# Kernel optimization log

Measured on AMD Instinct MI355X. Metric: run time of the kernel, lower is better.

## Reference

```python
import jax, jax.numpy as jnp
import numpy as np

# static architecture constants (match init_kwargs)
H, D, N_BASIS, MEM_LEN, QLEN = 16, 128, 1024, 512, 2048
RIDGE = 0.5
BASIS_SIGMAS = (0.005, 0.01)


def _gaussian_pdf(x, mu, sigma):
    return jnp.exp(-0.5 * ((x - mu) / sigma) ** 2) / (sigma * jnp.sqrt(2.0 * jnp.pi))


def _basis_params(n):
    # torch.meshgrid(linspace(0,1,n//2), sigmas, indexing='ij') then flatten
    m = jnp.linspace(0.0, 1.0, n // len(BASIS_SIGMAS)).astype(jnp.float32)
    mu = jnp.repeat(m, len(BASIS_SIGMAS))
    sigma = jnp.tile(jnp.asarray(BASIS_SIGMAS, jnp.float32), n // len(BASIS_SIGMAS))
    return mu, sigma


def _compute_G(l, b_mu, b_sigma, n):
    # padded linear positions on [-0.5+shift, 1.5-shift], l even -> 2l points
    shift = 1.0 / (2 * l)
    pos = jnp.linspace(-0.5 + shift, 1.5 - shift, 2 * l).astype(jnp.float32)
    F = _gaussian_pdf(pos[None, :], b_mu[:, None], b_sigma[:, None])  # [N, 2l]
    # G = F^T (F F^T + ridge I)^{-1}, then crop padding rows -> [l, N]
    G = jnp.linalg.solve(F @ F.T + RIDGE * jnp.eye(n, dtype=jnp.float32), F).T
    return G[l // 2: -(l // 2)]


def _forward(k, q, W_key, W_val, W_out, w_mu, w_sigma):
    d = H * D
    b_mu, b_sigma = _basis_params(N_BASIS)
    k = k[:, -512:, :]                                   # forward truncates memory
    l = k.shape[1]
    G = _compute_G(l, b_mu, b_sigma, N_BASIS)            # [l, N]
    # value_function: project signal onto basis coefficients B -> [1, N, d]
    B = jnp.einsum('bld,ln->bnd', k, G)
    keys = (B @ W_key.T).reshape(1, N_BASIS, H, D).transpose(0, 2, 1, 3)    # [1,H,N,D]
    values = (B @ W_val.T).reshape(1, N_BASIS, H, D).transpose(0, 2, 1, 3)  # [1,H,N,D]
    scores = jnp.einsum('bhqd,bhnd->bhqn', q / jnp.sqrt(jnp.float32(D)), keys)
    mu = jax.nn.sigmoid(scores @ w_mu)[..., None]                           # [1,H,Q,1]
    sigma_sq = jnp.maximum(jax.nn.softplus(scores @ w_sigma), 1e-4)[..., None]
    # continuous softmax over Gaussian RBFs: r_j = E_{t~N(mu,sigma_sq)}[psi_j(t)]
    # closed form: N(mu; b_mu_j, sigma_sq + b_sigma_j^2)
    r = _gaussian_pdf(b_mu, mu, jnp.sqrt(sigma_sq + b_sigma ** 2))          # [1,H,Q,N]
    context = jnp.einsum('bhqn,bhnd->bqhd', r, values).reshape(1, QLEN, d)
    return context @ W_out.T


def setup_inputs() -> dict:
    key = jax.random.key(0)
    ks = jax.random.split(key, 7)
    d = H * D
    s = 0.02
    return {
        'k': jax.random.normal(ks[0], (1, MEM_LEN, d), jnp.float32),
        'q': jax.random.normal(ks[1], (1, H, QLEN, D), jnp.float32),
        'W_key': jax.random.normal(ks[2], (d, d), jnp.float32) * s,
        'W_val': jax.random.normal(ks[3], (d, d), jnp.float32) * s,
        'W_out': jax.random.normal(ks[4], (d, d), jnp.float32) * s,
        'w_mu': jax.random.normal(ks[5], (N_BASIS,), jnp.float32) * s,
        'w_sigma': jax.random.normal(ks[6], (N_BASIS,), jnp.float32) * s,
        'new_doc': 1,
    }


def reference(k, q, W_key, W_val, W_out, w_mu, w_sigma, new_doc):
    # new_doc=True -> B_past/x_past reset, so only the fresh-memory path runs
    return _forward(k, q, W_key, W_val, W_out, w_mu, w_sigma)
```

## Files before the change

kernel.cpp:

```cpp
#include <hip/hip_runtime.h>
#include <hip/hip_bf16.h>
#include <vector>
#include <cmath>
#include <cstring>

using bf16 = __hip_bfloat16;
typedef short s16x8 __attribute__((ext_vector_type(8)));
typedef float f32x4 __attribute__((ext_vector_type(4)));

static constexpr int kH = 16, kD = 128, kNB = 1024, kML = 512, kQL = 2048, kDM = 2048;

#define VMB(N) do { asm volatile("s_waitcnt vmcnt(" #N ")" ::: "memory"); \
                    __builtin_amdgcn_s_barrier(); \
                    asm volatile("" ::: "memory"); } while (0)
#define VMLB(N) do { asm volatile("s_waitcnt vmcnt(" #N ") lgkmcnt(0)" ::: "memory"); \
                     __builtin_amdgcn_s_barrier(); \
                     asm volatile("" ::: "memory"); } while (0)
#define SWZ(c) ((c) ^ (((c) >> 4) & 3))

static void compute_Gt_host(float* Gt) {
  const int n = kNB, P = 2 * kML;
  std::vector<double> F((size_t)n * P), A((size_t)n * n), pos(P);
  const double shift = 1.0 / (double)P;
  const double p0 = -0.5 + shift, p1 = 1.5 - shift;
  for (int i = 0; i < P; i++) pos[i] = p0 + (p1 - p0) * (double)i / (double)(P - 1);
  const double c0 = 0.3989422804014327;
  std::vector<int> lo(n), hi(n);
  for (int b = 0; b < n; b++) {
    double mu = (double)(b >> 1) / 511.0;
    double sg = (b & 1) ? 0.01 : 0.005;
    double c = c0 / sg;
    double* Fb = &F[(size_t)b * P];
    for (int i = 0; i < P; i++) { double t = (pos[i] - mu) / sg; Fb[i] = c * exp(-0.5 * t * t); }
    int l = 0; while (l < P - 1 && pos[l] < mu - 14.0 * sg) l++;
    int h = P - 1; while (h > 0 && pos[h] > mu + 14.0 * sg) h--;
    lo[b] = l; hi[b] = h;
  }
  for (int i = 0; i < n; i++) {
    const double* fi = &F[(size_t)i * P];
    for (int j = 0; j <= i; j++) {
      const double* fj = &F[(size_t)j * P];
      int a = lo[i] > lo[j] ? lo[i] : lo[j];
      int b2 = hi[i] < hi[j] ? hi[i] : hi[j];
      double s = 0.0;
      for (int k2 = a; k2 <= b2; k2++) s += fi[k2] * fj[k2];
      A[(size_t)i * n + j] = s;
      if (i != j) A[(size_t)j * n + i] = s;
    }
    A[(size_t)i * n + i] += 0.5;
  }
  for (int j = 0; j < n; j++) {
    double* Aj = &A[(size_t)j * n];
    double d = Aj[j];
    for (int k2 = 0; k2 < j; k2++) d -= Aj[k2] * Aj[k2];
    d = std::sqrt(d); Aj[j] = d;
    double inv = 1.0 / d;
    for (int i = j + 1; i < n; i++) {
      double* Ai = &A[(size_t)i * n];
      double s = Ai[j];
      for (int k2 = 0; k2 < j; k2++) s -= Ai[k2] * Aj[k2];
      Ai[j] = s * inv;
    }
  }
  for (int i = 0; i < n; i++) {
    double* yi = &F[(size_t)i * P];
    const double* Ai = &A[(size_t)i * n];
    for (int k2 = 0; k2 < i; k2++) {
      double lik = Ai[k2];
      const double* yk = &F[(size_t)k2 * P];
      for (int t = 0; t < P; t++) yi[t] -= lik * yk[t];
    }
    double inv = 1.0 / Ai[i];
    for (int t = 0; t < P; t++) yi[t] *= inv;
  }
  for (int i = n - 1; i >= 0; i--) {
    double* xi = &F[(size_t)i * P];
    for (int k2 = i + 1; k2 < n; k2++) {
      double lki = A[(size_t)k2 * n + i];
      const double* xk = &F[(size_t)k2 * P];
      for (int t = 0; t < P; t++) xi[t] -= lki * xk[t];
    }
    double inv = 1.0 / A[(size_t)i * n + i];
    for (int t = 0; t < P; t++) xi[t] *= inv;
  }
  for (int b = 0; b < n; b++)
    for (int l = 0; l < kML; l++)
      Gt[(size_t)b * kML + l] = (float)F[(size_t)b * P + (kML / 2) + l];
}

static unsigned short f2bf_host(float x) {
  unsigned u; std::memcpy(&u, &x, 4);
  unsigned r = (u + 0x7FFFu + ((u >> 16) & 1u)) >> 16;
  return (unsigned short)r;
}
static float bf2f_host(unsigned short b) {
  unsigned u = ((unsigned)b) << 16; float f; std::memcpy(&f, &u, 4); return f;
}

namespace {
struct Init {
  float* d_GtTf = nullptr;
  unsigned short* d_Gth = nullptr;
  unsigned short* d_Gtl = nullptr;
  float* h_GtTf_pinned = nullptr;
  unsigned short* h_Gth_pinned = nullptr;
  unsigned short* h_Gtl_pinned = nullptr;
  std::vector<float> h_GtTf;
  std::vector<unsigned short> h_Gth, h_Gtl;
  Init() {
    std::vector<float> h_Gt((size_t)kNB * kML);
    compute_Gt_host(h_Gt.data());
    h_GtTf.resize(h_Gt.size());
    h_Gth.resize(h_Gt.size());
    h_Gtl.resize(h_Gt.size());
    for (int n = 0; n < kNB; n++)
      for (int l = 0; l < kML; l++) {
        float v = h_Gt[(size_t)n * kML + l];
        h_GtTf[(size_t)l * kNB + n] = v;
        unsigned short hb = f2bf_host(v);
        h_Gth[(size_t)n * kML + l] = hb;
        h_Gtl[(size_t)n * kML + l] = f2bf_host(v - bf2f_host(hb));
      }
    const size_t fb = h_Gt.size() * 4, bb = h_Gt.size() * 2;
    if (hipMalloc((void**)&d_GtTf, fb) == hipSuccess) {
      if (hipMemcpy(d_GtTf, h_GtTf.data(), fb, hipMemcpyHostToDevice) != hipSuccess) { hipFree(d_GtTf); d_GtTf = nullptr; }
    }
    if (hipMalloc((void**)&d_Gth, bb) == hipSuccess) {
      if (hipMemcpy(d_Gth, h_Gth.data(), bb, hipMemcpyHostToDevice) != hipSuccess) { hipFree(d_Gth); d_Gth = nullptr; }
    }
    if (hipMalloc((void**)&d_Gtl, bb) == hipSuccess) {
      if (hipMemcpy(d_Gtl, h_Gtl.data(), bb, hipMemcpyHostToDevice) != hipSuccess) { hipFree(d_Gtl); d_Gtl = nullptr; }
    }
    if (!d_GtTf && hipHostMalloc((void**)&h_GtTf_pinned, fb, 0) == hipSuccess)
      std::memcpy(h_GtTf_pinned, h_GtTf.data(), fb);
    if (!d_Gth && hipHostMalloc((void**)&h_Gth_pinned, bb, 0) == hipSuccess)
      std::memcpy(h_Gth_pinned, h_Gth.data(), bb);
    if (!d_Gtl && hipHostMalloc((void**)&h_Gtl_pinned, bb, 0) == hipSuccess)
      std::memcpy(h_Gtl_pinned, h_Gtl.data(), bb);
  }
};
Init g_init;
}

__device__ inline short f2bf(float x) {
  unsigned u = __float_as_uint(x);
  unsigned r = (u + 0x7FFFu + ((u >> 16) & 1u)) >> 16;
  return (short)r;
}
__device__ inline float bf2f(short b) {
  return __uint_as_float(((unsigned)(unsigned short)b) << 16);
}

__device__ inline void gload16(const void* g, void* l) {
  __builtin_amdgcn_global_load_lds(
      (__attribute__((address_space(1))) void*)(g),
      (__attribute__((address_space(3))) void*)(l),
      16, 0, 0);
}

__global__ __launch_bounds__(256) void detect_kernel(const unsigned short* __restrict__ q,
                                                     int* __restrict__ flag) {
  int t = threadIdx.x;
  int bad = 0;
  for (int i = t; i < 4096; i += 256) {
    int e = (q[i] >> 7) & 0xFF;
    if (e >= 0x98) bad = 1;
  }
  __shared__ int s[256];
  s[t] = bad; __syncthreads();
  for (int k2 = 128; k2 > 0; k2 >>= 1) { if (t < k2) s[t] |= s[t + k2]; __syncthreads(); }
  if (t == 0) *flag = s[0];
}

__global__ __launch_bounds__(256) void conv_bf16(const void* __restrict__ in,
                                                 short* __restrict__ out, int n4,
                                                 const int* __restrict__ flag) {
  int i = blockIdx.x * 256 + threadIdx.x;
  if (i >= n4) return;
  if (*flag) {
    float4 v = ((const float4*)in)[i];
    short4 o; o.x = f2bf(v.x); o.y = f2bf(v.y); o.z = f2bf(v.z); o.w = f2bf(v.w);
    ((short4*)out)[i] = o;
  } else {
    ((short4*)out)[i] = ((const short4*)in)[i];
  }
}

__global__ __launch_bounds__(256) void gw_kernel(const float* __restrict__ GtT,
                                                 const void* __restrict__ wmu,
                                                 const void* __restrict__ wsg,
                                                 float* __restrict__ gw,
                                                 const int* __restrict__ flag) {
  const bool f32 = (*flag != 0);
  const int l = blockIdx.x, t = threadIdx.x;
  const float* row = GtT + (long long)l * kNB;
  float a = 0.f, b = 0.f;
  for (int n = t; n < kNB; n += 256) {
    float g = row[n];
    float wm_ = f32 ? ((const float*)wmu)[n] : bf2f(((const short*)wmu)[n]);
    float ws_ = f32 ? ((const float*)wsg)[n] : bf2f(((const short*)wsg)[n]);
    a += g * wm_; b += g * ws_;
  }
  __shared__ float red[2][256];
  red[0][t] = a; red[1][t] = b;
  __syncthreads();
  for (int s = 128; s > 0; s >>= 1) {
    if (t < s) { red[0][t] += red[0][t + s]; red[1][t] += red[1][t + s]; }
    __syncthreads();
  }
  if (t == 0) { gw[l] = red[0][0]; gw[kML + l] = red[1][0]; }
}

__global__ __launch_bounds__(256) void bwk_kernel(const void* __restrict__ kin,
                                                  const float* __restrict__ gw,
                                                  float* __restrict__ bw,
                                                  const int* __restrict__ flag) {
  const bool f32 = (*flag != 0);
  int j = blockIdx.x * 256 + threadIdx.x;
  int l0 = blockIdx.y * 32;
  float a = 0.f, b = 0.f;
  for (int l = l0; l < l0 + 32; l++) {
    float kv = f32 ? ((const float*)kin)[(long long)l * kDM + j]
                   : bf2f(((const short*)kin)[(long long)l * kDM + j]);
    a += kv * gw[l]; b += kv * gw[kML + l];
  }
  atomicAdd(&bw[j], a);
  atomicAdd(&bw[kDM + j], b);
}

__global__ __launch_bounds__(256) void kw_kernel(const void* __restrict__ Wk,
                                                 const float* __restrict__ bw,
                                                 float* __restrict__ kw,
                                                 const int* __restrict__ flag) {
  const bool f32 = (*flag != 0);
  int i = blockIdx.x;
  float smu = 0.f, ssg = 0.f;
  if (f32) {
    const float* row = (const float*)Wk + (long long)i * kDM;
    for (int j = threadIdx.x; j < kDM; j += 256) { float w = row[j]; smu += w * bw[j]; ssg += w * bw[kDM + j]; }
  } else {
    const short* row = (const short*)Wk + (long long)i * kDM;
    for (int j = threadIdx.x; j < kDM; j += 256) { float w = bf2f(row[j]); smu += w * bw[j]; ssg += w * bw[kDM + j]; }
  }
  __shared__ float red[2][256];
  red[0][threadIdx.x] = smu; red[1][threadIdx.x] = ssg;
  __syncthreads();
  for (int s = 128; s > 0; s >>= 1) {
    if (threadIdx.x < (unsigned)s) {
      red[0][threadIdx.x] += red[0][threadIdx.x + s];
      red[1][threadIdx.x] += red[1][threadIdx.x + s];
    }
    __syncthreads();
  }
  if (threadIdx.x == 0) { kw[i] = red[0][0]; kw[kDM + i] = red[1][0]; }
}

__global__ __launch_bounds__(256) void musig_kernel(const void* __restrict__ q,
                                                    const float* __restrict__ kw,
                                                    float* __restrict__ mu,
                                                    float* __restrict__ sigsq,
                                                    const int* __restrict__ flag) {
  const bool f32 = (*flag != 0);
  int w = threadIdx.x >> 6, lane = threadIdx.x & 63;
  int idx = blockIdx.x * 4 + w;
  int h = idx >> 11;
  const float* kmu = kw + h * kD;
  const float* ksg = kw + kDM + h * kD;
  float q0, q1;
  if (f32) {
    const float* qrow = (const float*)q + (long long)idx * kD;
    q0 = qrow[lane]; q1 = qrow[lane + 64];
  } else {
    const short* qrow = (const short*)q + (long long)idx * kD;
    q0 = bf2f(qrow[lane]); q1 = bf2f(qrow[lane + 64]);
  }
  float a = q0 * kmu[lane] + q1 * kmu[lane + 64];
  float b = q0 * ksg[lane] + q1 * ksg[lane + 64];
  for (int s = 32; s > 0; s >>= 1) { a += __shfl_xor(a, s); b += __shfl_xor(b, s); }
  if (lane == 0) {
    const float inv_sqrt_d = 0.08838834764831845f;
    float zm = a * inv_sqrt_d, zs = b * inv_sqrt_d;
    mu[idx] = 1.f / (1.f + __expf(-zm));
    float sp = (zs > 20.f) ? zs : log1pf(__expf(zs));
    sigsq[idx] = fmaxf(sp, 1e-4f);
  }
}

template <int CSTORE>
__global__ __launch_bounds__(256) void mfma_gemm_bt(
    const short* __restrict__ A0, int lda, long long sA,
    const short* __restrict__ BT0, int ldb, long long sB,
    void* __restrict__ C0, int ldc, long long sC,
    int K, const int* __restrict__ flag) {
  __shared__ s16x8 lA[3][1024];
  __shared__ s16x8 lB[3][512];
  const short* A = A0 + (long long)blockIdx.z * sA;
  const short* BT = BT0 + (long long)blockIdx.z * sB;
  const int t = threadIdx.x;
  const int wave = t >> 6, lane = t & 63;
  const int quad = lane >> 4, l16 = lane & 15;
  const int wm = wave >> 1, wn = wave & 1;
  const int m0 = blockIdx.y * 128, n0 = blockIdx.x * 64;
  const int srow = lane & 15, skc = lane >> 4;
  auto stage = [&](int b, int kk) {
#pragma unroll
    for (int i = 0; i < 2; i++) {
      int sub = wave + i * 4;
      int m = sub * 16 + srow;
#pragma unroll
      for (int ks = 0; ks < 2; ks++)
        gload16(A + (long long)(m0 + m) * lda + kk + ks * 32 + skc * 8,
                &lA[b][ks * 512 + sub * 64]);
    }
    int mB = wave * 16 + srow;
#pragma unroll
    for (int ks = 0; ks < 2; ks++)
      gload16(BT + (long long)(n0 + mB) * ldb + kk + ks * 32 + skc * 8,
              &lB[b][ks * 256 + wave * 64]);
  };
  f32x4 acc[4][2];
  const f32x4 z = {0.f, 0.f, 0.f, 0.f};
#pragma unroll
  for (int i = 0; i < 4; i++)
#pragma unroll
    for (int j = 0; j < 2; j++) acc[i][j] = z;
  stage(0, 0);
  stage(1, 64);
  VMB(6);
  const int NT = K >> 6;
  int cur = 0, pf = 2;
  for (int tt = 0; tt < NT; ++tt) {
    const bool more = (tt + 2 < NT);
    if (more) stage(pf, (tt + 2) << 6);
#pragma unroll
    for (int ks = 0; ks < 2; ks++) {
      s16x8 af[4], bfr[2];
#pragma unroll
      for (int i = 0; i < 4; i++) af[i] = lA[cur][ks * 512 + (wm * 4 + i) * 64 + lane];
#pragma unroll
      for (int j = 0; j < 2; j++) bfr[j] = lB[cur][ks * 256 + (wn * 2 + j) * 64 + lane];
#pragma unroll
      for (int i = 0; i < 4; i++)
#pragma unroll
        for (int j = 0; j < 2; j++)
          acc[i][j] = __builtin_amdgcn_mfma_f32_16x16x32_bf16(af[i], bfr[j], acc[i][j], 0, 0, 0);
    }
    if (more) VMB(6); else VMB(0);
    cur = (cur == 2) ? 0 : cur + 1;
    pf = (pf == 2) ? 0 : pf + 1;
  }
  if (CSTORE == 0) {
    short* Cp = (short*)C0 + (long long)blockIdx.z * sC;
#pragma unroll
    for (int i = 0; i < 4; i++)
#pragma unroll
      for (int j = 0; j < 2; j++) {
        int gn = n0 + (wn * 2 + j) * 16 + l16;
#pragma unroll
        for (int rg = 0; rg < 4; rg++) {
          int gm = m0 + (wm * 4 + i) * 16 + quad * 4 + rg;
          Cp[(long long)gm * ldc + gn] = f2bf(acc[i][j][rg]);
        }
      }
  } else {
    if (*flag) {
      float* Cp = (float*)C0 + (long long)blockIdx.z * sC;
#pragma unroll
      for (int i = 0; i < 4; i++)
#pragma unroll
        for (int j = 0; j < 2; j++) {
          int gn = n0 + (wn * 2 + j) * 16 + l16;
#pragma unroll
          for (int rg = 0; rg < 4; rg++) {
            int gm = m0 + (wm * 4 + i) * 16 + quad * 4 + rg;
            Cp[(long long)gm * ldc + gn] = acc[i][j][rg];
          }
        }
    } else {
      short* Cp = (short*)C0 + (long long)blockIdx.z * sC;
#pragma unroll
      for (int i = 0; i < 4; i++)
#pragma unroll
        for (int j = 0; j < 2; j++) {
          int gn = n0 + (wn * 2 + j) * 16 + l16;
#pragma unroll
          for (int rg = 0; rg < 4; rg++) {
            int gm = m0 + (wm * 4 + i) * 16 + quad * 4 + rg;
            Cp[(long long)gm * ldc + gn] = f2bf(acc[i][j][rg]);
          }
        }
    }
  }
}

__global__ __launch_bounds__(256) void mfma_gemm_sk(
    const short* __restrict__ A0, int lda,
    const short* __restrict__ BT0, int ldb,
    float* __restrict__ P, int ldc) {
  __shared__ s16x8 lA[3][1024], lB[3][512];
  const int t = threadIdx.x;
  const int wave = t >> 6, lane = t & 63;
  const int quad = lane >> 4, l16 = lane & 15;
  const int wm = wave >> 1, wn = wave & 1;
  const int m0 = blockIdx.y * 128, n0 = blockIdx.x * 64;
  const int kbeg = blockIdx.z * 512;
  const int srow = lane & 15, skc = lane >> 4;
  auto stage = [&](int b, int kk) {
#pragma unroll
    for (int i = 0; i < 2; i++) {
      int sub = wave + i * 4;
      int m = sub * 16 + srow;
#pragma unroll
      for (int ks = 0; ks < 2; ks++)
        gload16(A0 + (long long)(m0 + m) * lda + kk + ks * 32 + skc * 8,
                &lA[b][ks * 512 + sub * 64]);
    }
    int mB = wave * 16 + srow;
#pragma unroll
    for (int ks = 0; ks < 2; ks++)
      gload16(BT0 + (long long)(n0 + mB) * ldb + kk + ks * 32 + skc * 8,
              &lB[b][ks * 256 + wave * 64]);
  };
  f32x4 acc[4][2];
  const f32x4 z = {0.f, 0.f, 0.f, 0.f};
#pragma unroll
  for (int i = 0; i < 4; i++)
#pragma unroll
    for (int j = 0; j < 2; j++) acc[i][j] = z;
  stage(0, kbeg);
  stage(1, kbeg + 64);
  VMB(6);
  const int NT = 8;
  int cur = 0, pf = 2;
  for (int tt = 0; tt < NT; ++tt) {
    const bool more = (tt + 2 < NT);
    if (more) stage(pf, kbeg + ((tt + 2) << 6));
#pragma unroll
    for (int ks = 0; ks < 2; ks++) {
      s16x8 af[4], bfr[2];
#pragma unroll
      for (int i = 0; i < 4; i++) af[i] = lA[cur][ks * 512 + (wm * 4 + i) * 64 + lane];
#pragma unroll
      for (int j = 0; j < 2; j++) bfr[j] = lB[cur][ks * 256 + (wn * 2 + j) * 64 + lane];
#pragma unroll
      for (int i = 0; i < 4; i++)
#pragma unroll
        for (int j = 0; j < 2; j++)
          acc[i][j] = __builtin_amdgcn_mfma_f32_16x16x32_bf16(af[i], bfr[j], acc[i][j], 0, 0, 0);
    }
    if (more) VMB(6); else VMB(0);
    cur = (cur == 2) ? 0 : cur + 1;
    pf = (pf == 2) ? 0 : pf + 1;
  }
  float* Cp = P + (long long)blockIdx.z * kML * kDM;
#pragma unroll
  for (int i = 0; i < 4; i++)
#pragma unroll
    for (int j = 0; j < 2; j++) {
      int gn = n0 + (wn * 2 + j) * 16 + l16;
#pragma unroll
      for (int rg = 0; rg < 4; rg++) {
        int gm = m0 + (wm * 4 + i) * 16 + quad * 4 + rg;
        Cp[(long long)gm * ldc + gn] = acc[i][j][rg];
      }
    }
}

__global__ __launch_bounds__(256) void reduceT_kernel(const float* __restrict__ P,
                                                      short* __restrict__ kvT) {
  __shared__ float tile[64][65];
  const int bd = blockIdx.x, bl = blockIdx.y;
  const int tx = threadIdx.x & 63, ty = threadIdx.x >> 6;
  for (int i = ty; i < 64; i += 4) {
    int l = bl * 64 + i, d = bd * 64 + tx;
    float s = 0.f;
#pragma unroll
    for (int z = 0; z < 4; z++) s += P[((long long)z * kML + l) * kDM + d];
    tile[i][tx] = s;
  }
  __syncthreads();
  for (int i = ty; i < 64; i += 4) {
    int d = bd * 64 + i, l = bl * 64 + tx;
    kvT[(long long)d * kML + l] = f2bf(tile[tx][i]);
  }
}

__global__ __launch_bounds__(256) void mfma_gemm_bt2(
    const short* __restrict__ A0, int lda,
    const short* __restrict__ BTh, const short* __restrict__ BTl, int ldb,
    short* __restrict__ Ch, short* __restrict__ Cl, int ldc, int K) {
  __shared__ s16x8 lA[3][256], lBh[3][256], lBl[3][256];
  const int t = threadIdx.x;
  const int wave = t >> 6, lane = t & 63;
  const int quad = lane >> 4, l16 = lane & 15;
  const int wm = wave >> 1, wn = wave & 1;
  const int m0 = blockIdx.y * 64, n0 = blockIdx.x * 64;
  const int srow = lane & 15, skc = lane >> 4;
  auto stage = [&](int b, int kk) {
    int m = wave * 16 + srow;
    gload16(A0 + (long long)(m0 + m) * lda + kk + skc * 8, &lA[b][wave * 64]);
    gload16(BTh + (long long)(n0 + m) * ldb + kk + skc * 8, &lBh[b][wave * 64]);
    gload16(BTl + (long long)(n0 + m) * ldb + kk + skc * 8, &lBl[b][wave * 64]);
  };
  f32x4 acc[2][2];
  const f32x4 z = {0.f, 0.f, 0.f, 0.f};
#pragma unroll
  for (int i = 0; i < 2; i++)
#pragma unroll
    for (int j = 0; j < 2; j++) acc[i][j] = z;
  stage(0, 0);
  stage(1, 32);
  VMB(3);
  const int NT = K >> 5;
  int cur = 0, pf = 2;
  for (int tt = 0; tt < NT; ++tt) {
    const bool more = (tt + 2 < NT);
    if (more) stage(pf, (tt + 2) << 5);
    s16x8 af[2], bh[2], bl[2];
#pragma unroll
    for (int i = 0; i < 2; i++) af[i] = lA[cur][(wm * 2 + i) * 64 + lane];
#pragma unroll
    for (int j = 0; j < 2; j++) {
      bh[j] = lBh[cur][(wn * 2 + j) * 64 + lane];
      bl[j] = lBl[cur][(wn * 2 + j) * 64 + lane];
    }
#pragma unroll
    for (int i = 0; i < 2; i++)
#pragma unroll
      for (int j = 0; j < 2; j++) {
        acc[i][j] = __builtin_amdgcn_mfma_f32_16x16x32_bf16(af[i], bh[j], acc[i][j], 0, 0, 0);
        acc[i][j] = __builtin_amdgcn_mfma_f32_16x16x32_bf16(af[i], bl[j], acc[i][j], 0, 0, 0);
      }
    if (more) VMB(3); else VMB(0);
    cur = (cur == 2) ? 0 : cur + 1;
    pf = (pf == 2) ? 0 : pf + 1;
  }
#pragma unroll
  for (int i = 0; i < 2; i++)
#pragma unroll
    for (int j = 0; j < 2; j++) {
      int gn = n0 + (wn * 2 + j) * 16 + l16;
#pragma unroll
      for (int rg = 0; rg < 4; rg++) {
        int gm = m0 + (wm * 2 + i) * 16 + quad * 4 + rg;
        float v = acc[i][j][rg];
        short hb = f2bf(v);
        Ch[(long long)gm * ldc + gn] = hb;
        Cl[(long long)gm * ldc + gn] = f2bf(v - bf2f(hb));
      }
    }
}

__global__ __launch_bounds__(256) void mfma_rv(
    const float* __restrict__ mu_all, const float* __restrict__ s2_all,
    const short* __restrict__ VTh, const short* __restrict__ VTl,
    short* __restrict__ ctx) {
  __shared__ s16x8 lAh[3][256], lAl[3][256], lBh[3][512], lBl[3][512];
  const int t = threadIdx.x;
  const int wave = t >> 6, lane = t & 63;
  const int quad = lane >> 4, l16 = lane & 15;
  const int wm = wave >> 1, wn = wave & 1;
  const int h = blockIdx.z;
  const int m0 = blockIdx.y * 64;
  const int r0 = t >> 2, kc = t & 3;
  const int srow = lane & 15, skc = lane >> 4;
  const long long voff = (long long)h * kD * kNB;
  const int row = h * kQL + m0 + r0;
  const float m_ = mu_all[row], s2 = s2_all[row];
  float ivs[2], cof[2];
  ivs[0] = rsqrtf(s2 + 2.5e-5f);
  ivs[1] = rsqrtf(s2 + 1e-4f);
  cof[0] = 0.3989422804014327f * ivs[0];
  cof[1] = 0.3989422804014327f * ivs[1];
  const int cidx = SWZ((r0 >> 4) * 64 + kc * 16 + (r0 & 15));
  auto stageB = [&](int b, int kk) {
#pragma unroll
    for (int i = 0; i < 2; i++) {
      int sub = wave + i * 4;
      int m = sub * 16 + srow;
      gload16(VTh + voff + (long long)m * kNB + kk + skc * 8, &lBh[b][sub * 64]);
      gload16(VTl + voff + (long long)m * kNB + kk + skc * 8, &lBl[b][sub * 64]);
    }
  };
  auto stageA = [&](int b, int kk) {
    s16x8 hv, lv;
#pragma unroll
    for (int jj = 0; jj < 8; jj++) {
      int n = kk + kc * 8 + jj;
      float bmu = (float)(n >> 1) * (1.f / 511.f);
      int p = jj & 1;
      float tt = (bmu - m_) * ivs[p];
      float v = cof[p] * __expf(-0.5f * tt * tt);
      short hb = f2bf(v);
      hv[jj] = hb;
      lv[jj] = f2bf(v - bf2f(hb));
    }
    lAh[b][cidx] = hv;
    lAl[b][cidx] = lv;
  };
  f32x4 acc[2][4];
  const f32x4 z = {0.f, 0.f, 0.f, 0.f};
#pragma unroll
  for (int i = 0; i < 2; i++)
#pragma unroll
    for (int j = 0; j < 4; j++) acc[i][j] = z;
  stageB(0, 0);
  stageA(0, 0);
  stageB(1, 32);
  stageA(1, 32);
  VMLB(4);
  const int NT = kNB >> 5;
  int cur = 0, pf = 2;
  for (int tt = 0; tt < NT; ++tt) {
    const bool more = (tt + 2 < NT);
    if (more) {
      stageB(pf, (tt + 2) << 5);
      stageA(pf, (tt + 2) << 5);
    }
    s16x8 ah[2], al[2], bh[4], bl[4];
#pragma unroll
    for (int i = 0; i < 2; i++) {
      ah[i] = lAh[cur][SWZ((wm * 2 + i) * 64 + lane)];
      al[i] = lAl[cur][SWZ((wm * 2 + i) * 64 + lane)];
    }
#pragma unroll
    for (int j = 0; j < 4; j++) {
      bh[j] = lBh[cur][(wn * 4 + j) * 64 + lane];
      bl[j] = lBl[cur][(wn * 4 + j) * 64 + lane];
    }
#pragma unroll
    for (int i = 0; i < 2; i++)
#pragma unroll
      for (int j = 0; j < 4; j++) {
        acc[i][j] = __builtin_amdgcn_mfma_f32_16x16x32_bf16(ah[i], bh[j], acc[i][j], 0, 0, 0);
        acc[i][j] = __builtin_amdgcn_mfma_f32_16x16x32_bf16(ah[i], bl[j], acc[i][j], 0, 0, 0);
        acc[i][j] = __builtin_amdgcn_mfma_f32_16x16x32_bf16(al[i], bh[j], acc[i][j], 0, 0, 0);
      }
    if (more) VMLB(4); else VMLB(0);
    cur = (cur == 2) ? 0 : cur + 1;
    pf = (pf == 2) ? 0 : pf + 1;
  }
  short* Cp = ctx + h * kD;
#pragma unroll
  for (int i = 0; i < 2; i++)
#pragma unroll
    for (int j = 0; j < 4; j++) {
      int gn = (wn * 4 + j) * 16 + l16;
#pragma unroll
      for (int rg = 0; rg < 4; rg++) {
        int gm = m0 + (wm * 2 + i) * 16 + quad * 4 + rg;
        Cp[(long long)gm * kDM + gn] = f2bf(acc[i][j][rg]);
      }
    }
}

extern "C" void kernel_launch(void* const* d_in, const int* in_sizes, int n_in,
                              void* d_out, int out_size, void* d_ws, size_t ws_size,
                              hipStream_t stream) {
  (void)in_sizes; (void)n_in; (void)out_size; (void)ws_size;
  const void* kmem = d_in[0];
  const void* q    = d_in[1];
  const void* Wk   = d_in[2];
  const void* Wv   = d_in[3];
  const void* Wo   = d_in[4];
  const void* wmu  = d_in[5];
  const void* wsg  = d_in[6];

  char* ws = (char*)d_ws;
  short* k_bf  = (short*)ws;
  short* kvT   = (short*)(ws + ((size_t)2 << 20));
  short* Wv_bf = (short*)(ws + ((size_t)4 << 20));
  short* Wo_bf = Wv_bf;
  float* Pbuf  = (float*)(ws + ((size_t)12 << 20));
  short* VTh   = (short*)(ws + ((size_t)12 << 20));
  short* VTl   = (short*)(ws + ((size_t)16 << 20));
  short* ctx   = (short*)(ws + ((size_t)20 << 20));
  float* tail  = (float*)(ws + ((size_t)28 << 20));
  float* gw    = tail;
  float* bw    = gw + 2 * kML;
  float* kw    = bw + 2 * kDM;
  float* mu    = kw + 2 * kDM;
  float* sigsq = mu + kH * kQL;
  int*   flag  = (int*)(sigsq + kH * kQL);
  float* gtffall = (float*)(ws + ((size_t)28 << 20) + ((size_t)1 << 19));
  short* ghfall  = (short*)(ws + ((size_t)30 << 20) + ((size_t)1 << 19));
  short* glfall  = (short*)(ws + ((size_t)31 << 20) + ((size_t)1 << 19));

  const float* GtTf = g_init.d_GtTf;
  if (!GtTf) {
    const void* src = g_init.h_GtTf_pinned ? (const void*)g_init.h_GtTf_pinned
                                           : (const void*)g_init.h_GtTf.data();
    hipMemcpyAsync(gtffall, src, (size_t)kNB * kML * 4, hipMemcpyHostToDevice, stream);
    GtTf = gtffall;
  }
  const short* Gh = (const short*)g_init.d_Gth;
  if (!Gh) {
    const void* src = g_init.h_Gth_pinned ? (const void*)g_init.h_Gth_pinned
                                          : (const void*)g_init.h_Gth.data();
    hipMemcpyAsync(ghfall, src, (size_t)kNB * kML * 2, hipMemcpyHostToDevice, stream);
    Gh = ghfall;
  }
  const short* Gl = (const short*)g_init.d_Gtl;
  if (!Gl) {
    const void* src = g_init.h_Gtl_pinned ? (const void*)g_init.h_Gtl_pinned
                                          : (const void*)g_init.h_Gtl.data();
    hipMemcpyAsync(glfall, src, (size_t)kNB * kML * 2, hipMemcpyHostToDevice, stream);
    Gl = glfall;
  }

  detect_kernel<<<1, 256, 0, stream>>>((const unsigned short*)q, flag);

  conv_bf16<<<(kML * kDM / 4 + 255) / 256, 256, 0, stream>>>(kmem, k_bf, kML * kDM / 4, flag);
  conv_bf16<<<(kDM * kDM / 4 + 255) / 256, 256, 0, stream>>>(Wv, Wv_bf, kDM * kDM / 4, flag);

  gw_kernel<<<kML, 256, 0, stream>>>(GtTf, wmu, wsg, gw, flag);
  hipMemsetAsync(bw, 0, 2 * kDM * sizeof(float), stream);
  bwk_kernel<<<dim3(kDM / 256, kML / 32), 256, 0, stream>>>(kmem, gw, bw, flag);
  kw_kernel<<<kDM, 256, 0, stream>>>(Wk, bw, kw, flag);
  musig_kernel<<<kH * kQL / 4, 256, 0, stream>>>(q, kw, mu, sigsq, flag);

  mfma_gemm_sk<<<dim3(kDM / 64, kML / 128, 4), 256, 0, stream>>>(
      k_bf, kDM, Wv_bf, kDM, Pbuf, kDM);
  reduceT_kernel<<<dim3(kDM / 64, kML / 64), 256, 0, stream>>>(Pbuf, kvT);

  conv_bf16<<<(kDM * kDM / 4 + 255) / 256, 256, 0, stream>>>(Wo, Wo_bf, kDM * kDM / 4, flag);

  mfma_gemm_bt2<<<dim3(kNB / 64, kDM / 64, 1), 256, 0, stream>>>(
      kvT, kML, Gh, Gl, kML, VTh, VTl, kNB, kML);

  mfma_rv<<<dim3(1, kQL / 64, kH), 256, 0, stream>>>(mu, sigsq, VTh, VTl, ctx);

  mfma_gemm_bt<2><<<dim3(kDM / 64, kQL / 128, 1), 256, 0, stream>>>(
      ctx, kDM, 0, Wo_bf, kDM, 0, d_out, kDM, 0, kDM, flag);
}
```

Measured before the change: 268.2 us.

## Fuse dtype detect with conversions, drop bw atomics, fold mu/sigma into rv kernel

Merges the dtype-detect kernel and the two bf16 conversion kernels into one prep kernel, where every block re-runs detection on a smaller 512-element sample of q. Rewrites bwk so each thread loops over all 512 memory rows and writes directly, which removes the memset and the atomics. Removes musig_kernel and computes mu and sigma_sq inside mfma_rv from q and kw. Launch count and intermediate traffic drop, but bwk now runs only 8 blocks with a long serial loop and each block repeats the detection work.

```diff
diff --git a/kernel.cpp b/kernel.cpp
--- a/kernel.cpp
+++ b/kernel.cpp
@@ -158,18 +158,39 @@
       16, 0, 0);
 }
 
-__global__ __launch_bounds__(256) void detect_kernel(const unsigned short* __restrict__ q,
-                                                     int* __restrict__ flag) {
-  int t = threadIdx.x;
+__device__ inline int detect_local(const unsigned short* q) {
   int bad = 0;
-  for (int i = t; i < 4096; i += 256) {
+  for (int i = threadIdx.x; i < 512; i += 256) {
     int e = (q[i] >> 7) & 0xFF;
     if (e >= 0x98) bad = 1;
   }
   __shared__ int s[256];
-  s[t] = bad; __syncthreads();
-  for (int k2 = 128; k2 > 0; k2 >>= 1) { if (t < k2) s[t] |= s[t + k2]; __syncthreads(); }
-  if (t == 0) *flag = s[0];
+  s[threadIdx.x] = bad; __syncthreads();
+  for (int k2 = 128; k2 > 0; k2 >>= 1) {
+    if (threadIdx.x < k2) s[threadIdx.x] |= s[threadIdx.x + k2];
+    __syncthreads();
+  }
+  return s[0];
+}
+
+__global__ __launch_bounds__(256) void prep_kernel(const unsigned short* __restrict__ q,
+                                                   const void* __restrict__ kin,
+                                                   const void* __restrict__ Wv,
+                                                   short* __restrict__ k_bf,
+                                                   short* __restrict__ Wv_bf,
+                                                   int* __restrict__ flag) {
+  const int f32 = detect_local(q);
+  if (blockIdx.x == 0 && threadIdx.x == 0) *flag = f32;
+  const void* src; short* dst; int i;
+  if (blockIdx.x < 1024) { src = kin; dst = k_bf; i = blockIdx.x * 256 + threadIdx.x; }
+  else { src = Wv; dst = Wv_bf; i = (blockIdx.x - 1024) * 256 + threadIdx.x; }
+  if (f32) {
+    float4 v = ((const float4*)src)[i];
+    short4 o; o.x = f2bf(v.x); o.y = f2bf(v.y); o.z = f2bf(v.z); o.w = f2bf(v.w);
+    ((short4*)dst)[i] = o;
+  } else {
+    ((short4*)dst)[i] = ((const short4*)src)[i];
+  }
 }
 
 __global__ __launch_bounds__(256) void conv_bf16(const void* __restrict__ in,
@@ -217,15 +238,15 @@
                                                   const int* __restrict__ flag) {
   const bool f32 = (*flag != 0);
   int j = blockIdx.x * 256 + threadIdx.x;
-  int l0 = blockIdx.y * 32;
   float a = 0.f, b = 0.f;
-  for (int l = l0; l < l0 + 32; l++) {
+#pragma unroll 4
+  for (int l = 0; l < kML; l++) {
     float kv = f32 ? ((const float*)kin)[(long long)l * kDM + j]
                    : bf2f(((const short*)kin)[(long long)l * kDM + j]);
     a += kv * gw[l]; b += kv * gw[kML + l];
   }
-  atomicAdd(&bw[j], a);
-  atomicAdd(&bw[kDM + j], b);
+  bw[j] = a;
+  bw[kDM + j] = b;
 }
 
 __global__ __launch_bounds__(256) void kw_kernel(const void* __restrict__ Wk,
@@ -253,37 +274,6 @@
     __syncthreads();
   }
   if (threadIdx.x == 0) { kw[i] = red[0][0]; kw[kDM + i] = red[1][0]; }
-}
-
-__global__ __launch_bounds__(256) void musig_kernel(const void* __restrict__ q,
-                                                    const float* __restrict__ kw,
-                                                    float* __restrict__ mu,
-                                                    float* __restrict__ sigsq,
-                                                    const int* __restrict__ flag) {
-  const bool f32 = (*flag != 0);
-  int w = threadIdx.x >> 6, lane = threadIdx.x & 63;
-  int idx = blockIdx.x * 4 + w;
-  int h = idx >> 11;
-  const float* kmu = kw + h * kD;
-  const float* ksg = kw + kDM + h * kD;
-  float q0, q1;
-  if (f32) {
-    const float* qrow = (const float*)q + (long long)idx * kD;
-    q0 = qrow[lane]; q1 = qrow[lane + 64];
-  } else {
-    const short* qrow = (const short*)q + (long long)idx * kD;
-    q0 = bf2f(qrow[lane]); q1 = bf2f(qrow[lane + 64]);
-  }
-  float a = q0 * kmu[lane] + q1 * kmu[lane + 64];
-  float b = q0 * ksg[lane] + q1 * ksg[lane + 64];
-  for (int s = 32; s > 0; s >>= 1) { a += __shfl_xor(a, s); b += __shfl_xor(b, s); }
-  if (lane == 0) {
-    const float inv_sqrt_d = 0.08838834764831845f;
-    float zm = a * inv_sqrt_d, zs = b * inv_sqrt_d;
-    mu[idx] = 1.f / (1.f + __expf(-zm));
-    float sp = (zs > 20.f) ? zs : log1pf(__expf(zs));
-    sigsq[idx] = fmaxf(sp, 1e-4f);
-  }
 }
 
 template <int CSTORE>
@@ -552,7 +542,8 @@
 }
 
 __global__ __launch_bounds__(256) void mfma_rv(
-    const float* __restrict__ mu_all, const float* __restrict__ s2_all,
+    const void* __restrict__ q, const float* __restrict__ kw,
+    const int* __restrict__ flag,
     const short* __restrict__ VTh, const short* __restrict__ VTl,
     short* __restrict__ ctx) {
   __shared__ s16x8 lAh[3][256], lAl[3][256], lBh[3][512], lBl[3][512];
@@ -566,23 +557,48 @@
   const int srow = lane & 15, skc = lane >> 4;
   const long long voff = (long long)h * kD * kNB;
   const int row = h * kQL + m0 + r0;
-  const float m_ = mu_all[row], s2 = s2_all[row];
+  float a = 0.f, b = 0.f;
+  {
+    const bool f32q = (*flag != 0);
+    const float* kmu = kw + h * kD;
+    const float* ksg = kw + kDM + h * kD;
+    if (f32q) {
+      const float* qrow = (const float*)q + (long long)row * kD;
+      for (int jj = kc * 32; jj < kc * 32 + 32; jj++) {
+        float qv = qrow[jj];
+        a += qv * kmu[jj]; b += qv * ksg[jj];
+      }
+    } else {
+      const short* qrow = (const short*)q + (long long)row * kD;
+      for (int jj = kc * 32; jj < kc * 32 + 32; jj++) {
+        float qv = bf2f(qrow[jj]);
+        a += qv * kmu[jj]; b += qv * ksg[jj];
+      }
+    }
+    a += __shfl_xor(a, 1); a += __shfl_xor(a, 2);
+    b += __shfl_xor(b, 1); b += __shfl_xor(b, 2);
+  }
+  const float inv_sqrt_d = 0.08838834764831845f;
+  const float zm = a * inv_sqrt_d, zs = b * inv_sqrt_d;
+  const float m_ = 1.f / (1.f + __expf(-zm));
+  const float sp = (zs > 20.f) ? zs : log1pf(__expf(zs));
+  const float s2 = fmaxf(sp, 1e-4f);
   float ivs[2], cof[2];
   ivs[0] = rsqrtf(s2 + 2.5e-5f);
   ivs[1] = rsqrtf(s2 + 1e-4f);
   cof[0] = 0.3989422804014327f * ivs[0];
   cof[1] = 0.3989422804014327f * ivs[1];
   const int cidx = SWZ((r0 >> 4) * 64 + kc * 16 + (r0 & 15));
-  auto stageB = [&](int b, int kk) {
+  auto stageB = [&](int bb, int kk) {
 #pragma unroll
     for (int i = 0; i < 2; i++) {
       int sub = wave + i * 4;
       int m = sub * 16 + srow;
-      gload16(VTh + voff + (long long)m * kNB + kk + skc * 8, &lBh[b][sub * 64]);
-      gload16(VTl + voff + (long long)m * kNB + kk + skc * 8, &lBl[b][sub * 64]);
+      gload16(VTh + voff + (long long)m * kNB + kk + skc * 8, &lBh[bb][sub * 64]);
+      gload16(VTl + voff + (long long)m * kNB + kk + skc * 8, &lBl[bb][sub * 64]);
     }
   };
-  auto stageA = [&](int b, int kk) {
+  auto stageA = [&](int bb, int kk) {
     s16x8 hv, lv;
 #pragma unroll
     for (int jj = 0; jj < 8; jj++) {
@@ -595,8 +611,8 @@
       hv[jj] = hb;
       lv[jj] = f2bf(v - bf2f(hb));
     }
-    lAh[b][cidx] = hv;
-    lAl[b][cidx] = lv;
+    lAh[bb][cidx] = hv;
+    lAl[bb][cidx] = lv;
   };
   f32x4 acc[2][4];
   const f32x4 z = {0.f, 0.f, 0.f, 0.f};
@@ -679,9 +695,7 @@
   float* gw    = tail;
   float* bw    = gw + 2 * kML;
   float* kw    = bw + 2 * kDM;
-  float* mu    = kw + 2 * kDM;
-  float* sigsq = mu + kH * kQL;
-  int*   flag  = (int*)(sigsq + kH * kQL);
+  int*   flag  = (int*)(kw + 2 * kDM);
   float* gtffall = (float*)(ws + ((size_t)28 << 20) + ((size_t)1 << 19));
   short* ghfall  = (short*)(ws + ((size_t)30 << 20) + ((size_t)1 << 19));
   short* glfall  = (short*)(ws + ((size_t)31 << 20) + ((size_t)1 << 19));
@@ -708,16 +722,12 @@
     Gl = glfall;
   }
 
-  detect_kernel<<<1, 256, 0, stream>>>((const unsigned short*)q, flag);
-
-  conv_bf16<<<(kML * kDM / 4 + 255) / 256, 256, 0, stream>>>(kmem, k_bf, kML * kDM / 4, flag);
-  conv_bf16<<<(kDM * kDM / 4 + 255) / 256, 256, 0, stream>>>(Wv, Wv_bf, kDM * kDM / 4, flag);
+  prep_kernel<<<5120, 256, 0, stream>>>((const unsigned short*)q, kmem, Wv,
+                                        k_bf, Wv_bf, flag);
 
   gw_kernel<<<kML, 256, 0, stream>>>(GtTf, wmu, wsg, gw, flag);
-  hipMemsetAsync(bw, 0, 2 * kDM * sizeof(float), stream);
-  bwk_kernel<<<dim3(kDM / 256, kML / 32), 256, 0, stream>>>(kmem, gw, bw, flag);
+  bwk_kernel<<<kDM / 256, 256, 0, stream>>>(kmem, gw, bw, flag);
   kw_kernel<<<kDM, 256, 0, stream>>>(Wk, bw, kw, flag);
-  musig_kernel<<<kH * kQL / 4, 256, 0, stream>>>(q, kw, mu, sigsq, flag);
 
   mfma_gemm_sk<<<dim3(kDM / 64, kML / 128, 4), 256, 0, stream>>>(
       k_bf, kDM, Wv_bf, kDM, Pbuf, kDM);
@@ -728,7 +738,7 @@
   mfma_gemm_bt2<<<dim3(kNB / 64, kDM / 64, 1), 256, 0, stream>>>(
       kvT, kML, Gh, Gl, kML, VTh, VTl, kNB, kML);
 
-  mfma_rv<<<dim3(1, kQL / 64, kH), 256, 0, stream>>>(mu, sigsq, VTh, VTl, ctx);
+  mfma_rv<<<dim3(1, kQL / 64, kH), 256, 0, stream>>>(q, kw, flag, VTh, VTl, ctx);
 
   mfma_gemm_bt<2><<<dim3(kDM / 64, kQL / 128, 1), 256, 0, stream>>>(
       ctx, kDM, 0, Wo_bf, kDM, 0, d_out, kDM, 0, kDM, flag);
```

After: 305.2 us. 1.14x slower.
